# Performance work log

Hardware: AMD Instinct MI355X
Metric: run time of the kernel (lower is better)

## Reference

```python
import jax, jax.numpy as jnp
import numpy as np

BLOCK = 4  # block_size from init_kwargs


def space_to_channel_3d(x, b):
    # Faithful translation of SpaceToChannel_3d.forward (torch split/stack/permute chain).
    B, C, W, H, D = x.shape
    y = x.transpose(0, 2, 3, 4, 1)                      # (B, W, H, D, C)
    y = y.reshape(B, W, H, D // b, b, C)                # split depth into D//b chunks of b
    y = y.transpose(0, 3, 1, 2, 4, 5)                   # (B, D//b, W, H, b, C)
    y = y.reshape(B, D // b, W // b, H // b, C * b * b * b)  # per-chunk row-major reshape
    y = y.transpose(0, 2, 3, 1, 4)                      # (B, W//b, H//b, D//b, C*b^3)
    return y.transpose(0, 4, 1, 2, 3)                   # (B, C*b^3, W//b, H//b, D//b)


def channel_to_space_3d(x, b):
    # Faithful translation of ChannelToSpace_3d.forward.
    B, Cd, wd, hd, dd = x.shape
    b3 = b * b * b
    Cs = Cd // b3
    y = x.transpose(0, 2, 3, 4, 1)                      # (B, wd, hd, dd, Cd)
    y = y.reshape(B, wd, hd, dd, b * b, b, Cs)          # split b^3 dim into b^2 chunks of b
    y = y.transpose(0, 4, 1, 2, 3, 5, 6)                # (B, b^2, wd, hd, dd, b, Cs)
    y = y.reshape(B, b * b, wd, hd, dd * b, Cs)         # merge (dd, b) per chunk
    y = y.transpose(0, 2, 1, 3, 4, 5)                   # (B, wd, b^2, hd, dd*b, Cs)
    y = y.reshape(B, wd * b, hd * b, dd * b, Cs)        # row-major merge of (wd, b^2, hd)
    return y.transpose(0, 4, 1, 2, 3)                   # (B, Cs, wd*b, hd*b, dd*b)


def setup_inputs() -> dict:
    key = jax.random.key(0)
    k1, k2 = jax.random.split(key)
    x = jax.random.normal(k1, (4, 32, 64, 64, 64), dtype=jnp.float32)
    gamma = jax.random.normal(k2, (1,), dtype=jnp.float32)
    return {"x": x, "gamma": gamma}


def reference(x, gamma):
    b = BLOCK
    y = space_to_channel_3d(x, b)                       # (B, C*b^3, w, h, d)
    B, C, w, h, d = y.shape
    q = y.reshape(B, C, w * h * d)                      # (B, C', N)
    # channel-wise attention: energy (B, C', C')
    energy = jnp.einsum('bcn,ben->bce', q, q)
    energy_new = jnp.max(energy, axis=-1, keepdims=True) - energy
    attention = jax.nn.softmax(energy_new, axis=-1)
    out = jnp.einsum('bce,ben->bcn', attention, q)      # (B, C', N)
    out = out.reshape(B, C, w, h, d)
    out = gamma * out + y
    return channel_to_space_3d(out, b)
```

## Files before the change

kernel.cpp:

```cpp
#include <hip/hip_runtime.h>

typedef _Float16 f16;
typedef __attribute__((ext_vector_type(8))) _Float16 f16x8;
typedef __attribute__((ext_vector_type(4))) float f32x4;

#define CCH 2048
#define NSP 4096
#define NB  4

#define VMCNT8 asm volatile("s_waitcnt vmcnt(8)" ::: "memory")
#define VMCNT4 asm volatile("s_waitcnt vmcnt(4)" ::: "memory")
#define VMCNT0 asm volatile("s_waitcnt vmcnt(0)" ::: "memory")
#define CFENCE asm volatile("" ::: "memory")

__device__ __forceinline__ void gld16(const void* g, void* l) {
  __builtin_amdgcn_global_load_lds(
      (const __attribute__((address_space(1))) void*)g,
      (__attribute__((address_space(3))) void*)l, 16, 0, 0);
}

__global__ void pack_kernel(const float* __restrict__ x, f16* __restrict__ qh,
                            f16* __restrict__ ql, int b0) {
  int gid = blockIdx.x * 256 + threadIdx.x;
  int n = gid & (NSP - 1);
  int t = gid >> 12;
  int c = t & 31; t >>= 5;
  int r = t & 15; int ib = t >> 4;
  int wc = n >> 8, hc = (n >> 4) & 15, dc = n & 15;
  int w = wc * 4 + (hc >> 2);
  int h = (hc & 3) * 16 + r;
  int b = b0 + ib;
  const f32x4 v = *(const f32x4*)(x + ((((size_t)b * 32 + c) * 64 + w) * 64 + h) * 64 + dc * 4);
#pragma unroll
  for (int bd = 0; bd < 4; ++bd) {
    int cc = r * 128 + bd * 32 + c;
    size_t o = ((size_t)ib * CCH + cc) * NSP + n;
    float val = v[bd];
    f16 hi = (f16)val;
    qh[o] = hi;
    ql[o] = (f16)(val - (float)hi);
  }
}

__global__ void transpose_kernel(const f16* __restrict__ qh, f16* __restrict__ qhT) {
  int ib = blockIdx.z;
  int j0 = blockIdx.x * 64, n0 = blockIdx.y * 64;
  __shared__ f16 tile[64][72];
  int t = threadIdx.x;
  int r = t >> 3;
  int cb = (t & 7) * 8;
#pragma unroll
  for (int half = 0; half < 2; ++half) {
    int rr = r + half * 32;
    f16x8 v = *(const f16x8*)(qh + ((size_t)ib * CCH + j0 + rr) * NSP + n0 + cb);
    *(f16x8*)&tile[rr][cb] = v;
  }
  __syncthreads();
#pragma unroll
  for (int half = 0; half < 2; ++half) {
    int rr = r + half * 32;
    f16x8 o;
#pragma unroll
    for (int u = 0; u < 8; ++u) o[u] = tile[cb + u][rr];
    *(f16x8*)(qhT + ((size_t)ib * NSP + n0 + rr) * CCH + j0 + cb) = o;
  }
}

__global__ __launch_bounds__(256) void gemm1_kernel(const f16* __restrict__ qh,
                                                    const f16* __restrict__ ql,
                                                    float* __restrict__ energy,
                                                    int ksplit) {
  int ib = blockIdx.z;
  int nwg = gridDim.x;
  int cpx = nwg >> 3;
  int bx = blockIdx.x;
  int tri = (bx & 7) * cpx + (bx >> 3);
  int ks = 0;
  if (ksplit == 2) { ks = tri >= 136; tri -= ks * 136; }
  int rem = tri, bi = 0, span = 16;
  while (rem >= span) { rem -= span; ++bi; --span; }
  int bj = bi + rem;
  int i0 = bi * 128, j0 = bj * 128;
  int kbeg = ks * 2048;
  int kend = (ksplit == 2) ? kbeg + 2048 : NSP;
  float* eout = energy + ((size_t)(ks * gridDim.z + ib)) * CCH * CCH;

  __shared__ f16 Lds[2][4][128 * 32];
  int tid = threadIdx.x;
  int lane = tid & 63, wv = tid >> 6;
  int l15 = lane & 15, quad = lane >> 4;
  int wr = (wv >> 1) * 64, wcol = (wv & 1) * 64;
  int swz = (l15 >> 1) & 3;
  int kbs = (lane & 3) ^ ((lane >> 3) & 3);

  const f16* srcA = (wv & 1) ? ql : qh;
  int rbase = (wv < 2) ? i0 : j0;
  const f16* gsrc = srcA + ((size_t)ib * CCH + rbase) * NSP
                    + (size_t)(lane >> 2) * NSP + kbs * 8;

  auto stage = [&](int buf, int kk) {
    f16* ld = &Lds[buf][wv][0];
#pragma unroll
    for (int t = 0; t < 8; ++t)
      gld16(gsrc + (size_t)(t * 16) * NSP + kk, ld + t * 512);
  };

  const f32x4 vzero = {0.f, 0.f, 0.f, 0.f};
  f32x4 acc[4][4];
#pragma unroll
  for (int a = 0; a < 4; ++a)
#pragma unroll
    for (int bq = 0; bq < 4; ++bq) acc[a][bq] = vzero;

  int nk = (kend - kbeg) >> 5;
  stage(0, kbeg);
  __syncthreads();
  for (int it = 0; it < nk; ++it) {
    int cur = it & 1;
    if (it + 1 < nk) stage(cur ^ 1, kbeg + ((it + 1) << 5));
    f16x8 ah[4], al[4], bh[4], bl[4];
#pragma unroll
    for (int mt = 0; mt < 4; ++mt) {
      int row = wr + mt * 16 + l15;
      ah[mt] = *(const f16x8*)&Lds[cur][0][row * 32 + ((quad ^ swz) * 8)];
      al[mt] = *(const f16x8*)&Lds[cur][1][row * 32 + ((quad ^ swz) * 8)];
    }
#pragma unroll
    for (int nt = 0; nt < 4; ++nt) {
      int col = wcol + nt * 16 + l15;
      bh[nt] = *(const f16x8*)&Lds[cur][2][col * 32 + ((quad ^ swz) * 8)];
      bl[nt] = *(const f16x8*)&Lds[cur][3][col * 32 + ((quad ^ swz) * 8)];
    }
    __builtin_amdgcn_s_setprio(1);
#pragma unroll
    for (int mt = 0; mt < 4; ++mt)
#pragma unroll
      for (int nt = 0; nt < 4; ++nt) {
        acc[mt][nt] = __builtin_amdgcn_mfma_f32_16x16x32_f16(ah[mt], bh[nt], acc[mt][nt], 0, 0, 0);
        acc[mt][nt] = __builtin_amdgcn_mfma_f32_16x16x32_f16(ah[mt], bl[nt], acc[mt][nt], 0, 0, 0);
        acc[mt][nt] = __builtin_amdgcn_mfma_f32_16x16x32_f16(al[mt], bh[nt], acc[mt][nt], 0, 0, 0);
      }
    __builtin_amdgcn_s_setprio(0);
    __syncthreads();
  }
  bool diag = (bi == bj);
#pragma unroll
  for (int mt = 0; mt < 4; ++mt)
#pragma unroll
    for (int nt = 0; nt < 4; ++nt)
#pragma unroll
      for (int rg = 0; rg < 4; ++rg) {
        int row = i0 + wr + mt * 16 + quad * 4 + rg;
        int col = j0 + wcol + nt * 16 + l15;
        float v = acc[mt][nt][rg];
        eout[(size_t)row * CCH + col] = v;
        if (!diag) eout[(size_t)col * CCH + row] = v;
      }
}

__global__ void softmax_kernel(const float* __restrict__ e0, const float* __restrict__ e1,
                               int two, const float* __restrict__ gamma_p,
                               f16* __restrict__ attn) {
  int i = blockIdx.x, ib = blockIdx.y;
  const float* r0 = e0 + ((size_t)ib * CCH + i) * CCH;
  const float* r1 = e1 + ((size_t)ib * CCH + i) * CCH;
  f16* arow = attn + ((size_t)ib * CCH + i) * CCH;
  int t = threadIdx.x;
  f32x4 v0 = *(const f32x4*)(r0 + t * 8);
  f32x4 v1 = *(const f32x4*)(r0 + t * 8 + 4);
  if (two) {
    f32x4 u0 = *(const f32x4*)(r1 + t * 8);
    f32x4 u1 = *(const f32x4*)(r1 + t * 8 + 4);
#pragma unroll
    for (int u = 0; u < 4; ++u) { v0[u] += u0[u]; v1[u] += u1[u]; }
  }
  float m = v0[0];
#pragma unroll
  for (int u = 1; u < 4; ++u) m = fminf(m, v0[u]);
#pragma unroll
  for (int u = 0; u < 4; ++u) m = fminf(m, v1[u]);
#pragma unroll
  for (int off = 32; off > 0; off >>= 1) m = fminf(m, __shfl_xor(m, off));
  __shared__ float redA[4], redB[4];
  if ((t & 63) == 0) redA[t >> 6] = m;
  __syncthreads();
  m = fminf(fminf(redA[0], redA[1]), fminf(redA[2], redA[3]));
  float e[8], s = 0.f;
#pragma unroll
  for (int u = 0; u < 4; ++u) { e[u] = __expf(m - v0[u]); s += e[u]; }
#pragma unroll
  for (int u = 0; u < 4; ++u) { e[4 + u] = __expf(m - v1[u]); s += e[4 + u]; }
#pragma unroll
  for (int off = 32; off > 0; off >>= 1) s += __shfl_xor(s, off);
  if ((t & 63) == 0) redB[t >> 6] = s;
  __syncthreads();
  s = redB[0] + redB[1] + redB[2] + redB[3];
  float gamma = *gamma_p;
  float ginv = gamma / s;
  int du = i - t * 8;
  f16x8 o;
#pragma unroll
  for (int u = 0; u < 8; ++u) {
    float v = e[u] * ginv;
    if (u == du) v += 1.0f;
    o[u] = (f16)v;
  }
  *(f16x8*)(arow + t * 8) = o;
}

__global__ __launch_bounds__(256) void gemm2_kernel(const f16* __restrict__ attn,
                                                    const f16* __restrict__ qhT,
                                                    float* __restrict__ out, int b0) {
  int ib = blockIdx.z;
  int lin = blockIdx.x + gridDim.x * blockIdx.y;
  int nwg = gridDim.x * gridDim.y;
  int cpx = nwg >> 3;
  int lin2 = (lin & 7) * cpx + (lin >> 3);
  int i0 = (lin2 & 15) * 128;
  int n0 = (lin2 >> 4) * 128;
  __shared__ f16 Lds[4][2][128 * 32];
  int tid = threadIdx.x;
  int lane = tid & 63, wv = tid >> 6;
  int l15 = lane & 15, quad = lane >> 4;
  int wr = (wv >> 1) * 64, wcol = (wv & 1) * 64;
  int swz = (l15 >> 1) & 3;
  int kbs = (lane & 3) ^ ((lane >> 3) & 3);

  int arr = wv >> 1, rh = wv & 1;
  const f16* gbase = arr ? (qhT + ((size_t)ib * NSP + n0) * CCH)
                         : (attn + ((size_t)ib * CCH + i0) * CCH);
  const f16* gsrc = gbase + (size_t)(rh * 64 + (lane >> 2)) * CCH + kbs * 8;

  auto stage = [&](int slot, int kk) {
#pragma unroll
    for (int t = 0; t < 4; ++t)
      gld16(gsrc + (size_t)(t * 16) * CCH + kk,
            &Lds[slot][arr][(rh * 64 + t * 16) * 32]);
  };

  const f32x4 vzero = {0.f, 0.f, 0.f, 0.f};
  f32x4 acc[4][4];
#pragma unroll
  for (int a = 0; a < 4; ++a)
#pragma unroll
    for (int bq = 0; bq < 4; ++bq) acc[a][bq] = vzero;

  const int NP = CCH / 32;
  stage(0, 0); stage(1, 32); stage(2, 64);
  for (int p = 0; p < NP; ++p) {
    int remp = NP - 1 - p;
    if (remp >= 2) { VMCNT8; } else if (remp == 1) { VMCNT4; } else { VMCNT0; }
    __builtin_amdgcn_s_barrier();
    CFENCE;
    if (p + 3 < NP) stage((p + 3) & 3, (p + 3) << 5);
    int s = p & 3;
    const f16* As = &Lds[s][0][0];
    const f16* Bs = &Lds[s][1][0];
    f16x8 af[4], bf[4];
#pragma unroll
    for (int mt = 0; mt < 4; ++mt)
      af[mt] = *(const f16x8*)&As[(wr + mt * 16 + l15) * 32 + ((quad ^ swz) * 8)];
#pragma unroll
    for (int nt = 0; nt < 4; ++nt)
      bf[nt] = *(const f16x8*)&Bs[(wcol + nt * 16 + l15) * 32 + ((quad ^ swz) * 8)];
    __builtin_amdgcn_s_setprio(1);
#pragma unroll
    for (int mt = 0; mt < 4; ++mt)
#pragma unroll
      for (int nt = 0; nt < 4; ++nt)
        acc[mt][nt] = __builtin_amdgcn_mfma_f32_16x16x32_f16(af[mt], bf[nt], acc[mt][nt], 0, 0, 0);
    __builtin_amdgcn_s_setprio(0);
  }

  __syncthreads();
  float* eld = (float*)&Lds[0][0][0];
#pragma unroll
  for (int mt = 0; mt < 4; ++mt) {
    int f = (wr >> 5) + (mt >> 1);
    int gb = (mt & 1) * 16 + quad * 4;
#pragma unroll
    for (int nt = 0; nt < 4; ++nt) {
      int jh = (wcol >> 4) + nt;
#pragma unroll
      for (int rg = 0; rg < 4; ++rg)
        eld[(gb + rg) * 512 + jh * 64 + l15 * 4 + f] = acc[mt][nt][rg];
    }
  }
  __syncthreads();
  int b = b0 + ib;
  int e = i0 >> 7;
  int iw = n0 >> 8;
  int W = iw * 4 + (e >> 2);
  int H0 = (e & 3) * 16 + ((n0 >> 4) & 15);
#pragma unroll
  for (int u = 0; u < 8; ++u) {
    int g = wv * 8 + u;
    size_t goff = ((((size_t)b * 32 + g) * 64 + W) * 4096) + (size_t)H0 * 64;
#pragma unroll
    for (int hv = 0; hv < 2; ++hv) {
      int fo = hv * 256 + lane * 4;
      *(f32x4*)(out + goff + fo) = *(const f32x4*)&eld[g * 512 + fo];
    }
  }
}

extern "C" void kernel_launch(void* const* d_in, const int* in_sizes, int n_in,
                              void* d_out, int out_size, void* d_ws, size_t ws_size,
                              hipStream_t stream) {
  const float* x = (const float*)d_in[0];
  const float* gamma = (const float*)d_in[1];
  float* out = (float*)d_out;

  const size_t szQ = (size_t)CCH * NSP;
  const size_t szE = (size_t)CCH * CCH;

  const size_t pbSplit = szQ * 2 * 3 + szE * 4 * 2 + szE * 2;
  const size_t pbNoSplit = szQ * 2 * 3 + szE * 4 + szE * 2;

  int ksplit, nb;
  if (ws_size >= (size_t)NB * pbSplit) { ksplit = 2; nb = NB; }
  else if (ws_size >= (size_t)NB * pbNoSplit) { ksplit = 1; nb = NB; }
  else { ksplit = 1; nb = 1; }

  char* p = (char*)d_ws;
  f16* qh = (f16*)p;   p += (size_t)nb * szQ * 2;
  f16* ql = (f16*)p;   p += (size_t)nb * szQ * 2;
  f16* qhT = (f16*)p;  p += (size_t)nb * szQ * 2;
  float* energy = (float*)p; p += (size_t)nb * szE * 4 * ksplit;
  f16* attn = (f16*)p;
  const float* e1 = (ksplit == 2) ? (energy + (size_t)nb * szE) : energy;

  for (int b0 = 0; b0 < NB; b0 += nb) {
    pack_kernel<<<nb * 8192, 256, 0, stream>>>(x, qh, ql, b0);
    transpose_kernel<<<dim3(32, 64, nb), 256, 0, stream>>>(qh, qhT);
    gemm1_kernel<<<dim3(136 * ksplit, 1, nb), 256, 0, stream>>>(qh, ql, energy, ksplit);
    softmax_kernel<<<dim3(CCH, nb), 256, 0, stream>>>(energy, e1, ksplit - 1, gamma, attn);
    gemm2_kernel<<<dim3(16, 32, nb), 256, 0, stream>>>(attn, qhT, out, b0);
  }
}
```

Measured before the change: 728.7 us.

## Fold split-precision correction terms into one combined operand, drop K-split

Replaces the low-order residual operand with v = 2x - hi so the energy product needs two fp16 MFMAs per tile instead of three, scaling the result by one half. Also removes the optional K-split path and its second energy buffer, so softmax reads a single energy matrix. This reduces matrix-core work and energy traffic but halves the gemm1 grid when the split was active, which may lower occupancy, and slightly changes rounding behaviour of the compensated product.

```diff
diff --git a/kernel.cpp b/kernel.cpp
--- a/kernel.cpp
+++ b/kernel.cpp
@@ -20,7 +20,7 @@
 }
 
 __global__ void pack_kernel(const float* __restrict__ x, f16* __restrict__ qh,
-                            f16* __restrict__ ql, int b0) {
+                            f16* __restrict__ qv, int b0) {
   int gid = blockIdx.x * 256 + threadIdx.x;
   int n = gid & (NSP - 1);
   int t = gid >> 12;
@@ -38,7 +38,7 @@
     float val = v[bd];
     f16 hi = (f16)val;
     qh[o] = hi;
-    ql[o] = (f16)(val - (float)hi);
+    qv[o] = (f16)(2.0f * val - (float)hi);
   }
 }
 
@@ -67,23 +67,16 @@
 }
 
 __global__ __launch_bounds__(256) void gemm1_kernel(const f16* __restrict__ qh,
-                                                    const f16* __restrict__ ql,
-                                                    float* __restrict__ energy,
-                                                    int ksplit) {
+                                                    const f16* __restrict__ qv,
+                                                    float* __restrict__ energy) {
   int ib = blockIdx.z;
-  int nwg = gridDim.x;
-  int cpx = nwg >> 3;
   int bx = blockIdx.x;
-  int tri = (bx & 7) * cpx + (bx >> 3);
-  int ks = 0;
-  if (ksplit == 2) { ks = tri >= 136; tri -= ks * 136; }
+  int tri = (bx & 7) * 17 + (bx >> 3);
   int rem = tri, bi = 0, span = 16;
   while (rem >= span) { rem -= span; ++bi; --span; }
   int bj = bi + rem;
   int i0 = bi * 128, j0 = bj * 128;
-  int kbeg = ks * 2048;
-  int kend = (ksplit == 2) ? kbeg + 2048 : NSP;
-  float* eout = energy + ((size_t)(ks * gridDim.z + ib)) * CCH * CCH;
+  float* eout = energy + (size_t)ib * CCH * CCH;
 
   __shared__ f16 Lds[2][4][128 * 32];
   int tid = threadIdx.x;
@@ -93,7 +86,7 @@
   int swz = (l15 >> 1) & 3;
   int kbs = (lane & 3) ^ ((lane >> 3) & 3);
 
-  const f16* srcA = (wv & 1) ? ql : qh;
+  const f16* srcA = (wv & 1) ? qv : qh;
   int rbase = (wv < 2) ? i0 : j0;
   const f16* gsrc = srcA + ((size_t)ib * CCH + rbase) * NSP
                     + (size_t)(lane >> 2) * NSP + kbs * 8;
@@ -112,33 +105,32 @@
 #pragma unroll
     for (int bq = 0; bq < 4; ++bq) acc[a][bq] = vzero;
 
-  int nk = (kend - kbeg) >> 5;
-  stage(0, kbeg);
+  const int nk = NSP >> 5;
+  stage(0, 0);
   __syncthreads();
   for (int it = 0; it < nk; ++it) {
     int cur = it & 1;
-    if (it + 1 < nk) stage(cur ^ 1, kbeg + ((it + 1) << 5));
-    f16x8 ah[4], al[4], bh[4], bl[4];
+    if (it + 1 < nk) stage(cur ^ 1, (it + 1) << 5);
+    f16x8 ah[4], av[4], bh[4], bv[4];
 #pragma unroll
     for (int mt = 0; mt < 4; ++mt) {
       int row = wr + mt * 16 + l15;
       ah[mt] = *(const f16x8*)&Lds[cur][0][row * 32 + ((quad ^ swz) * 8)];
-      al[mt] = *(const f16x8*)&Lds[cur][1][row * 32 + ((quad ^ swz) * 8)];
+      av[mt] = *(const f16x8*)&Lds[cur][1][row * 32 + ((quad ^ swz) * 8)];
     }
 #pragma unroll
     for (int nt = 0; nt < 4; ++nt) {
       int col = wcol + nt * 16 + l15;
       bh[nt] = *(const f16x8*)&Lds[cur][2][col * 32 + ((quad ^ swz) * 8)];
-      bl[nt] = *(const f16x8*)&Lds[cur][3][col * 32 + ((quad ^ swz) * 8)];
+      bv[nt] = *(const f16x8*)&Lds[cur][3][col * 32 + ((quad ^ swz) * 8)];
     }
     __builtin_amdgcn_s_setprio(1);
 #pragma unroll
     for (int mt = 0; mt < 4; ++mt)
 #pragma unroll
       for (int nt = 0; nt < 4; ++nt) {
-        acc[mt][nt] = __builtin_amdgcn_mfma_f32_16x16x32_f16(ah[mt], bh[nt], acc[mt][nt], 0, 0, 0);
-        acc[mt][nt] = __builtin_amdgcn_mfma_f32_16x16x32_f16(ah[mt], bl[nt], acc[mt][nt], 0, 0, 0);
-        acc[mt][nt] = __builtin_amdgcn_mfma_f32_16x16x32_f16(al[mt], bh[nt], acc[mt][nt], 0, 0, 0);
+        acc[mt][nt] = __builtin_amdgcn_mfma_f32_16x16x32_f16(ah[mt], bv[nt], acc[mt][nt], 0, 0, 0);
+        acc[mt][nt] = __builtin_amdgcn_mfma_f32_16x16x32_f16(av[mt], bh[nt], acc[mt][nt], 0, 0, 0);
       }
     __builtin_amdgcn_s_setprio(0);
     __syncthreads();
@@ -152,28 +144,21 @@
       for (int rg = 0; rg < 4; ++rg) {
         int row = i0 + wr + mt * 16 + quad * 4 + rg;
         int col = j0 + wcol + nt * 16 + l15;
-        float v = acc[mt][nt][rg];
+        float v = 0.5f * acc[mt][nt][rg];
         eout[(size_t)row * CCH + col] = v;
         if (!diag) eout[(size_t)col * CCH + row] = v;
       }
 }
 
-__global__ void softmax_kernel(const float* __restrict__ e0, const float* __restrict__ e1,
-                               int two, const float* __restrict__ gamma_p,
+__global__ void softmax_kernel(const float* __restrict__ e0,
+                               const float* __restrict__ gamma_p,
                                f16* __restrict__ attn) {
   int i = blockIdx.x, ib = blockIdx.y;
   const float* r0 = e0 + ((size_t)ib * CCH + i) * CCH;
-  const float* r1 = e1 + ((size_t)ib * CCH + i) * CCH;
   f16* arow = attn + ((size_t)ib * CCH + i) * CCH;
   int t = threadIdx.x;
   f32x4 v0 = *(const f32x4*)(r0 + t * 8);
   f32x4 v1 = *(const f32x4*)(r0 + t * 8 + 4);
-  if (two) {
-    f32x4 u0 = *(const f32x4*)(r1 + t * 8);
-    f32x4 u1 = *(const f32x4*)(r1 + t * 8 + 4);
-#pragma unroll
-    for (int u = 0; u < 4; ++u) { v0[u] += u0[u]; v1[u] += u1[u]; }
-  }
   float m = v0[0];
 #pragma unroll
   for (int u = 1; u < 4; ++u) m = fminf(m, v0[u]);
@@ -314,27 +299,22 @@
   const size_t szQ = (size_t)CCH * NSP;
   const size_t szE = (size_t)CCH * CCH;
 
-  const size_t pbSplit = szQ * 2 * 3 + szE * 4 * 2 + szE * 2;
-  const size_t pbNoSplit = szQ * 2 * 3 + szE * 4 + szE * 2;
-
-  int ksplit, nb;
-  if (ws_size >= (size_t)NB * pbSplit) { ksplit = 2; nb = NB; }
-  else if (ws_size >= (size_t)NB * pbNoSplit) { ksplit = 1; nb = NB; }
-  else { ksplit = 1; nb = 1; }
+  const size_t pb = szQ * 2 * 3 + szE * 4 + szE * 2;
+
+  int nb = (ws_size >= (size_t)NB * pb) ? NB : 1;
 
   char* p = (char*)d_ws;
   f16* qh = (f16*)p;   p += (size_t)nb * szQ * 2;
-  f16* ql = (f16*)p;   p += (size_t)nb * szQ * 2;
+  f16* qv = (f16*)p;   p += (size_t)nb * szQ * 2;
   f16* qhT = (f16*)p;  p += (size_t)nb * szQ * 2;
-  float* energy = (float*)p; p += (size_t)nb * szE * 4 * ksplit;
+  float* energy = (float*)p; p += (size_t)nb * szE * 4;
   f16* attn = (f16*)p;
-  const float* e1 = (ksplit == 2) ? (energy + (size_t)nb * szE) : energy;
 
   for (int b0 = 0; b0 < NB; b0 += nb) {
-    pack_kernel<<<nb * 8192, 256, 0, stream>>>(x, qh, ql, b0);
+    pack_kernel<<<nb * 8192, 256, 0, stream>>>(x, qh, qv, b0);
     transpose_kernel<<<dim3(32, 64, nb), 256, 0, stream>>>(qh, qhT);
-    gemm1_kernel<<<dim3(136 * ksplit, 1, nb), 256, 0, stream>>>(qh, ql, energy, ksplit);
-    softmax_kernel<<<dim3(CCH, nb), 256, 0, stream>>>(energy, e1, ksplit - 1, gamma, attn);
+    gemm1_kernel<<<dim3(136, 1, nb), 256, 0, stream>>>(qh, qv, energy);
+    softmax_kernel<<<dim3(CCH, nb), 256, 0, stream>>>(energy, gamma, attn);
     gemm2_kernel<<<dim3(16, 32, nb), 256, 0, stream>>>(attn, qhT, out, b0);
   }
 }
```

Measured after the change: 765.7 us. +5.1%, slower.
